# Kernel tuning notes

Measured on AMD Instinct MI355X. Metric: run time of the kernel, lower is better.

The kernel has to match this reference:

```python
import jax, jax.numpy as jnp
import numpy as np

D = 800  # embed dim == GRU units (hardcoded in module)


def gru_scan(x, h0, W, U, b):
    """Keras GRU, reset_after=True, activation=tanh, recurrent_activation=softmax.
    x: [B,T,D_in], h0: [B,H], W: [D_in,3H], U: [H,3H], b: [2,3H] (input bias, recurrent bias).
    Gate order: z, r, h (Keras convention). Returns (seq [B,T,H], last state [B,H])."""
    H = h0.shape[-1]
    # Precompute input projections for all timesteps (big fused GEMM).
    xg = jnp.einsum('btd,dk->btk', x, W) + b[0]          # [B,T,3H]
    xg = jnp.swapaxes(xg, 0, 1)                          # [T,B,3H]
    br = b[1]

    def step(h, xt):
        rec = h @ U + br                                 # [B,3H]
        rz, rr, rh = rec[:, :H], rec[:, H:2 * H], rec[:, 2 * H:]
        xz, xr, xh = xt[:, :H], xt[:, H:2 * H], xt[:, 2 * H:]
        z = jax.nn.softmax(xz + rz, axis=-1)             # recurrent_activation='softmax'
        r = jax.nn.softmax(xr + rr, axis=-1)
        hh = jnp.tanh(xh + r * rh)                       # reset_after: r applied after recurrent matmul
        hn = z * h + (1.0 - z) * hh
        return hn, hn

    hT, ys = jax.lax.scan(step, h0, xg)
    return jnp.swapaxes(ys, 0, 1), hT


def setup_inputs() -> dict:
    key = jax.random.key(0)
    ks = jax.random.split(key, 16)
    Vf, Ve, B, T = 30000, 32000, 64, 48
    s = 0.05

    def n(k, shape):
        return jax.random.normal(k, shape, jnp.float32) * s

    return {
        'encoder_input': jax.random.randint(ks[0], (B, T), 0, Vf),
        'decoder_input': jax.random.randint(ks[1], (B, T), 0, Ve),
        'emb_fr': n(ks[2], (Vf, D)),
        'W_d1': n(ks[3], (D, D)), 'b_d1': jnp.zeros((D,), jnp.float32),
        'Wf1': n(ks[4], (D, 3 * D)), 'Uf1': n(ks[5], (D, 3 * D)), 'bf1': jnp.zeros((2, 3 * D), jnp.float32),
        'Wf2': n(ks[6], (D, 3 * D)), 'Uf2': n(ks[7], (D, 3 * D)), 'bf2': jnp.zeros((2, 3 * D), jnp.float32),
        'emb_en': n(ks[8], (Ve, D)),
        'We1': n(ks[9], (D, 3 * D)), 'Ue1': n(ks[10], (D, 3 * D)), 'be1': jnp.zeros((2, 3 * D), jnp.float32),
        'We2': n(ks[11], (D, 3 * D)), 'Ue2': n(ks[12], (D, 3 * D)), 'be2': jnp.zeros((2, 3 * D), jnp.float32),
        'W_out': n(ks[13], (D, Ve)), 'b_out': jnp.zeros((Ve,), jnp.float32),
    }


def reference(encoder_input, decoder_input, emb_fr, W_d1, b_d1,
              Wf1, Uf1, bf1, Wf2, Uf2, bf2, emb_en,
              We1, Ue1, be1, We2, Ue2, be2, W_out, b_out):
    fe = emb_fr[encoder_input]                           # [B,Tf,D]
    fe = jax.nn.relu(fe @ W_d1 + b_d1)
    ee = emb_en[decoder_input]                           # [B,Te,D]
    B = encoder_input.shape[0]
    h0 = jnp.zeros((B, D), dtype=fe.dtype)
    g1, h1 = gru_scan(fe, h0, Wf1, Uf1, bf1)
    g2, h2 = gru_scan(g1, h1, Wf2, Uf2, bf2)
    e1, h3 = gru_scan(ee, h2, We1, Ue1, be1)
    e2, h4 = gru_scan(e1, h3, We2, Ue2, be2)
    logits = e2 @ W_out + b_out                          # [B,Te,Ve]
    return jax.nn.softmax(logits, axis=-1)
```

## Files before the change

### kernel.cpp

```cpp
#include <hip/hip_runtime.h>

#define DD 800
#define HH 800
#define BB 64
#define TT 48
#define N3H 2400
#define VV 32000
#define MR (TT*BB)
#define NBLK 25

typedef __attribute__((ext_vector_type(8))) short bf16x8;
typedef __attribute__((ext_vector_type(4))) float f32x4;
typedef __attribute__((ext_vector_type(4))) float float4v;
typedef __attribute__((address_space(1))) const unsigned int as1_uint;
typedef __attribute__((address_space(3))) unsigned int as3_uint;

__device__ __forceinline__ short f2bf(float f) {
  unsigned int u = __builtin_bit_cast(unsigned int, f);
  u = (u + 0x7fffu + ((u >> 16) & 1u)) >> 16;
  return (short)(unsigned short)u;
}

__device__ __forceinline__ void gload16(const void* g, void* l) {
  __builtin_amdgcn_global_load_lds((as1_uint*)g, (as3_uint*)l, 16, 0, 0);
}

__device__ __forceinline__ void store16_cc(short* p, bf16x8 v) {
  asm volatile("global_store_dwordx4 %0, %1, off sc0 sc1" :: "v"(p), "v"(v));
}

__global__ void k_cast_transpose(const float* __restrict__ src, short* __restrict__ dst,
                                 int K, int N) {
  __shared__ float tile[32][33];
  int n0 = blockIdx.x * 32, k0 = blockIdx.y * 32;
  int tx = threadIdx.x, ty = threadIdx.y;
#pragma unroll
  for (int i = 0; i < 4; ++i) {
    int k = k0 + ty + i * 8, n = n0 + tx;
    if (k < K && n < N) tile[ty + i * 8][tx] = src[(size_t)k * N + n];
  }
  __syncthreads();
#pragma unroll
  for (int i = 0; i < 4; ++i) {
    int n = n0 + ty + i * 8, k = k0 + tx;
    if (n < N && k < K) dst[(size_t)n * K + k] = f2bf(tile[tx][ty + i * 8]);
  }
}

__global__ void k_gather(const int* __restrict__ ids, const float* __restrict__ emb,
                         short* __restrict__ out) {
  int r = blockIdx.x;
  int t = r >> 6, b = r & 63;
  int id = ids[b * TT + t];
  int i = threadIdx.x;
  if (i < 100) {
    const float* s = emb + (size_t)id * DD + i * 8;
    float4v v0 = *(const float4v*)s;
    float4v v1 = *(const float4v*)(s + 4);
    bf16x8 o;
    o[0] = f2bf(v0[0]); o[1] = f2bf(v0[1]); o[2] = f2bf(v0[2]); o[3] = f2bf(v0[3]);
    o[4] = f2bf(v1[0]); o[5] = f2bf(v1[1]); o[6] = f2bf(v1[2]); o[7] = f2bf(v1[3]);
    *(bf16x8*)(out + (size_t)r * DD + i * 8) = o;
  }
}

template <int EPI>
__global__ __launch_bounds__(256) void k_gemm(const short* __restrict__ A,
                                              const short* __restrict__ BT,
                                              const float* __restrict__ bias,
                                              float* __restrict__ Cf,
                                              short* __restrict__ Cb,
                                              float* __restrict__ Pp,
                                              int N, int K, int ldc) {
  __shared__ short lA[128 * 32];
  __shared__ short lB[128 * 32];
  const int tid = threadIdx.x, wid = tid >> 6, lane = tid & 63;
  const int m0 = blockIdx.y * 128, n0 = blockIdx.x * 128;
  const int wr = wid >> 1, wc = wid & 1;
  f32x4 acc[4][4] = {};
  for (int kt = 0; kt < K / 32; ++kt) {
    const int kb = kt * 32;
#pragma unroll
    for (int rr = 0; rr < 2; ++rr) {
      int s = rr * 256 + tid;
      gload16(A + (size_t)(m0 + (s >> 2)) * K + kb + (s & 3) * 8, (char*)lA + s * 16);
      gload16(BT + (size_t)(n0 + (s >> 2)) * K + kb + (s & 3) * 8, (char*)lB + s * 16);
    }
    __syncthreads();
    bf16x8 af[4], bfr[4];
#pragma unroll
    for (int i = 0; i < 4; ++i)
      af[i] = *(const bf16x8*)(lA + (wr * 64 + i * 16 + (lane & 15)) * 32 + (lane >> 4) * 8);
#pragma unroll
    for (int j = 0; j < 4; ++j)
      bfr[j] = *(const bf16x8*)(lB + (wc * 64 + j * 16 + (lane & 15)) * 32 + (lane >> 4) * 8);
#pragma unroll
    for (int i = 0; i < 4; ++i)
#pragma unroll
      for (int j = 0; j < 4; ++j)
        acc[i][j] = __builtin_amdgcn_mfma_f32_16x16x32_bf16(af[i], bfr[j], acc[i][j], 0, 0, 0);
    __syncthreads();
  }
  const int hi = lane >> 4, ccol = lane & 15;
  if (EPI == 2) {
#pragma unroll
    for (int i = 0; i < 4; ++i) {
      int row = m0 + wr * 64 + i * 16 + hi * 4;
#pragma unroll
      for (int rg = 0; rg < 4; ++rg) {
        int r = row + rg;
        int orow = (r & 63) * TT + (r >> 6);
        float part = 0.f;
#pragma unroll
        for (int j = 0; j < 4; ++j) {
          int col = n0 + wc * 64 + j * 16 + ccol;
          float v = __expf(acc[i][j][rg] + bias[col]);
          part += v;
          Cf[(size_t)orow * ldc + col] = v;
        }
#pragma unroll
        for (int mm = 1; mm < 16; mm <<= 1) part += __shfl_xor(part, mm);
        if (ccol == 0) Pp[(size_t)orow * 512 + blockIdx.x * 2 + wc] = part;
      }
    }
  } else {
#pragma unroll
    for (int i = 0; i < 4; ++i) {
      int row = m0 + wr * 64 + i * 16 + hi * 4;
#pragma unroll
      for (int j = 0; j < 4; ++j) {
        int col = n0 + wc * 64 + j * 16 + ccol;
        if (col >= N) continue;
        float bv = bias ? bias[col] : 0.f;
#pragma unroll
        for (int rg = 0; rg < 4; ++rg) {
          int r = row + rg;
          float v = acc[i][j][rg] + bv;
          if (EPI == 0) Cf[(size_t)r * ldc + col] = v;
          else          Cb[(size_t)r * ldc + col] = f2bf(v < 0.f ? 0.f : v);
        }
      }
    }
  }
}

__device__ __forceinline__ void bar_sync(int* flags, int ep, int tid) {
  asm volatile("s_waitcnt vmcnt(0)" ::: "memory");
  __syncthreads();
  if (tid == 0)
    __hip_atomic_store(&flags[blockIdx.x * 32], ep, __ATOMIC_RELAXED, __HIP_MEMORY_SCOPE_AGENT);
  if (tid < 64) {
    bool ok;
    do {
      int v = ep;
      if (tid < NBLK)
        v = __hip_atomic_load(&flags[tid * 32], __ATOMIC_RELAXED, __HIP_MEMORY_SCOPE_AGENT);
      ok = __all(v - ep >= 0);
      if (!ok) __builtin_amdgcn_s_sleep(1);
    } while (!ok);
  }
  __syncthreads();
}

__global__ __launch_bounds__(512, 1) void k_scan(const float* __restrict__ xg,
                                                 const short* __restrict__ UT,
                                                 const float* __restrict__ br,
                                                 float* __restrict__ hF,
                                                 const short* __restrict__ hInit,
                                                 short* __restrict__ hSeq,
                                                 float* __restrict__ Spart,
                                                 int* flags, int ep0) {
  __shared__ short uT[96 * 808];
  __shared__ float sSum[128];
  __shared__ short hTile[64 * 32];
  const int tid = threadIdx.x, wid = tid >> 6, lane = tid & 63;
  const int bid = blockIdx.x, c0 = bid * 32;
  const int rt = wid & 3, ch = wid >> 2;
  for (int idx = tid; idx < 96 * 100; idx += 512) {
    int rr = idx / 100, chk = idx % 100;
    int grow = (rr >> 5) * HH + c0 + (rr & 31);
    *(bf16x8*)(uT + rr * 808 + chk * 8) = *(const bf16x8*)(UT + (size_t)grow * HH + chk * 8);
  }
  const int hi = lane >> 4;
  const int ccol = lane & 15;
  const int crow = rt * 16 + hi * 4;
  const int gcol = c0 + ch * 16 + ccol;
  const int arow = rt * 16 + ccol;
  const short* uz = uT + (0 * 32 + ch * 16 + ccol) * 808;
  const short* ur = uT + (1 * 32 + ch * 16 + ccol) * 808;
  const short* uh = uT + (2 * 32 + ch * 16 + ccol) * 808;
  f32x4 hfr;
#pragma unroll
  for (int rg = 0; rg < 4; ++rg) hfr[rg] = hF[(crow + rg) * HH + gcol];
  const float brz = br[gcol], brr = br[HH + gcol], brh = br[2 * HH + gcol];
  int ep = ep0;
  float xzv[4], xrv[4], xhv[4];
#pragma unroll
  for (int rg = 0; rg < 4; ++rg) {
    const float* xrow = xg + ((size_t)(crow + rg)) * N3H;
    xzv[rg] = xrow[gcol];
    xrv[rg] = xrow[HH + gcol];
    xhv[rg] = xrow[2 * HH + gcol];
  }
  __syncthreads();

#pragma unroll 1
  for (int t = 0; t < TT; ++t) {
    const short* hPrev = (t == 0) ? hInit : hSeq + (size_t)(t - 1) * BB * HH;
    bf16x8 areg[25];
#pragma unroll
    for (int kt = 0; kt < 25; ++kt)
      areg[kt] = *(const bf16x8*)(hPrev + arow * HH + kt * 32 + hi * 8);
    f32x4 az = {}, ar = {}, ah = {};
#pragma unroll
    for (int kt = 0; kt < 25; ++kt) {
      const int o = kt * 32 + hi * 8;
      az = __builtin_amdgcn_mfma_f32_16x16x32_bf16(areg[kt], *(const bf16x8*)(uz + o), az, 0, 0, 0);
      ar = __builtin_amdgcn_mfma_f32_16x16x32_bf16(areg[kt], *(const bf16x8*)(ur + o), ar, 0, 0, 0);
      ah = __builtin_amdgcn_mfma_f32_16x16x32_bf16(areg[kt], *(const bf16x8*)(uh + o), ah, 0, 0, 0);
    }
    float ez[4], er[4], rh[4];
    float* sb = Spart + (size_t)t * 50 * 128;
#pragma unroll
    for (int rg = 0; rg < 4; ++rg) {
      ez[rg] = __expf(xzv[rg] + az[rg] + brz);
      er[rg] = __expf(xrv[rg] + ar[rg] + brr);
      rh[rg] = ah[rg] + brh;
      float s1 = ez[rg], s2 = er[rg];
#pragma unroll
      for (int mm = 1; mm < 16; mm <<= 1) {
        s1 += __shfl_xor(s1, mm);
        s2 += __shfl_xor(s2, mm);
      }
      if (ccol == 0) {
        const int slot = bid * 2 + ch;
        __hip_atomic_store(&sb[slot * 128 + crow + rg], s1, __ATOMIC_RELAXED, __HIP_MEMORY_SCOPE_AGENT);
        __hip_atomic_store(&sb[slot * 128 + 64 + crow + rg], s2, __ATOMIC_RELAXED, __HIP_MEMORY_SCOPE_AGENT);
      }
    }
    bar_sync(flags, ++ep, tid);
    if (tid < 128) {
      float s = 0.f;
#pragma unroll
      for (int sl = 0; sl < 2 * NBLK; ++sl)
        s += __hip_atomic_load(&sb[sl * 128 + tid], __ATOMIC_RELAXED, __HIP_MEMORY_SCOPE_AGENT);
      sSum[tid] = s;
    }
    __syncthreads();
#pragma unroll
    for (int rg = 0; rg < 4; ++rg) {
      int r = crow + rg;
      float z = ez[rg] / sSum[r];
      float rr2 = er[rg] / sSum[64 + r];
      float hh = tanhf(xhv[rg] + rr2 * rh[rg]);
      float hn = z * hfr[rg] + (1.f - z) * hh;
      hfr[rg] = hn;
      hTile[r * 32 + ch * 16 + ccol] = f2bf(hn);
    }
    __syncthreads();
    short* hCur = hSeq + (size_t)t * BB * HH;
    if (tid < 256) {
      int row = tid >> 2, seg = tid & 3;
      store16_cc(hCur + row * HH + c0 + seg * 8, *(const bf16x8*)(hTile + row * 32 + seg * 8));
    }
    if (t + 1 < TT) {
#pragma unroll
      for (int rg = 0; rg < 4; ++rg) {
        const float* xrow = xg + ((size_t)(t + 1) * BB + crow + rg) * N3H;
        xzv[rg] = xrow[gcol];
        xrv[rg] = xrow[HH + gcol];
        xhv[rg] = xrow[2 * HH + gcol];
      }
    }
    bar_sync(flags, ++ep, tid);
  }
#pragma unroll
  for (int rg = 0; rg < 4; ++rg) hF[(crow + rg) * HH + gcol] = hfr[rg];
}

__global__ __launch_bounds__(256) void k_softmax(float* __restrict__ out,
                                                 const float* __restrict__ Pp) {
  float* row = out + (size_t)blockIdx.x * VV;
  const float* pp = Pp + (size_t)blockIdx.x * 512;
  const int tid = threadIdx.x;
  __shared__ float red[4];
  float sum = 0.f;
  for (int i = tid; i < 500; i += 256) sum += pp[i];
#pragma unroll
  for (int s = 32; s >= 1; s >>= 1) sum += __shfl_xor(sum, s);
  if ((tid & 63) == 0) red[tid >> 6] = sum;
  __syncthreads();
  float inv = 1.f / (red[0] + red[1] + red[2] + red[3]);
  for (int i = tid * 4; i < VV; i += 1024) {
    float4v v = *(const float4v*)(row + i);
    v[0] *= inv; v[1] *= inv; v[2] *= inv; v[3] *= inv;
    *(float4v*)(row + i) = v;
  }
}

extern "C" void kernel_launch(void* const* d_in, const int* in_sizes, int n_in,
                              void* d_out, int out_size, void* d_ws, size_t ws_size,
                              hipStream_t stream) {
  (void)in_sizes; (void)n_in; (void)out_size; (void)ws_size;
  const int*   enc  = (const int*)d_in[0];
  const int*   dec  = (const int*)d_in[1];
  const float* embF = (const float*)d_in[2];
  const float* Wd1  = (const float*)d_in[3];
  const float* bd1  = (const float*)d_in[4];
  const float* Wf1  = (const float*)d_in[5];
  const float* Uf1  = (const float*)d_in[6];
  const float* bf1  = (const float*)d_in[7];
  const float* Wf2  = (const float*)d_in[8];
  const float* Uf2  = (const float*)d_in[9];
  const float* bf2  = (const float*)d_in[10];
  const float* embE = (const float*)d_in[11];
  const float* We1  = (const float*)d_in[12];
  const float* Ue1  = (const float*)d_in[13];
  const float* be1  = (const float*)d_in[14];
  const float* We2  = (const float*)d_in[15];
  const float* Ue2  = (const float*)d_in[16];
  const float* be2  = (const float*)d_in[17];
  const float* Wout = (const float*)d_in[18];
  const float* bout = (const float*)d_in[19];

  char* p = (char*)d_ws;
  auto alloc = [&](size_t bytes) { char* r = p; p += (bytes + 255) & ~(size_t)255; return r; };
  short* WdT = (short*)alloc((size_t)896 * 800 * 2);
  short* WTb[4]; short* UTb[4];
  for (int i = 0; i < 4; ++i) {
    WTb[i] = (short*)alloc((size_t)2432 * 800 * 2);
    UTb[i] = (short*)alloc((size_t)2400 * 800 * 2);
  }
  short* WoT = (short*)alloc((size_t)VV * 800 * 2);
  short* feA = (short*)alloc((size_t)MR * DD * 2);
  short* fe  = (short*)alloc((size_t)MR * DD * 2);
  short* ee  = (short*)alloc((size_t)MR * DD * 2);
  short* g1  = (short*)alloc((size_t)MR * HH * 2);
  short* g2s = (short*)alloc((size_t)MR * HH * 2);
  short* e1  = (short*)alloc((size_t)MR * HH * 2);
  short* e2  = (short*)alloc((size_t)MR * HH * 2);
  float* xg  = (float*)alloc((size_t)MR * N3H * 4);
  float* Ppart = (float*)alloc((size_t)MR * 512 * 4);
  float* Spart = (float*)alloc((size_t)TT * 50 * 128 * 4);
  float* hF   = (float*)alloc((size_t)BB * HH * 4);
  short* hIn0 = (short*)alloc((size_t)BB * HH * 2);
  int* flags  = (int*)alloc((size_t)NBLK * 32 * 4);

  size_t tail = (char*)(flags + NBLK * 32) - (char*)hF;
  hipMemsetAsync(hF, 0, tail, stream);

  dim3 tb(32, 8);
  k_cast_transpose<<<dim3(25, 25), tb, 0, stream>>>(Wd1, WdT, 800, 800);
  const float* Ws[4] = {Wf1, Wf2, We1, We2};
  const float* Us[4] = {Uf1, Uf2, Ue1, Ue2};
  for (int i = 0; i < 4; ++i) {
    k_cast_transpose<<<dim3(75, 25), tb, 0, stream>>>(Ws[i], WTb[i], 800, 2400);
    k_cast_transpose<<<dim3(75, 25), tb, 0, stream>>>(Us[i], UTb[i], 800, 2400);
  }
  k_cast_transpose<<<dim3(1000, 25), tb, 0, stream>>>(Wout, WoT, 800, VV);
  k_gather<<<MR, 128, 0, stream>>>(enc, embF, feA);
  k_gather<<<MR, 128, 0, stream>>>(dec, embE, ee);
  k_gemm<1><<<dim3(7, 24), 256, 0, stream>>>(feA, WdT, bd1, nullptr, fe, nullptr, 800, 800, 800);

  const float* bs[4] = {bf1, bf2, be1, be2};
  const short* Xs[4] = {fe, g1, ee, e1};
  short* hSeqL[4] = {g1, g2s, e1, e2};
  for (int l = 0; l < 4; ++l) {
    const short* hInit = (l == 0) ? hIn0 : hSeqL[l - 1] + (size_t)(TT - 1) * BB * HH;
    k_gemm<0><<<dim3(19, 24), 256, 0, stream>>>(Xs[l], WTb[l], bs[l], xg, nullptr, nullptr, N3H, 800, N3H);
    k_scan<<<NBLK, 512, 0, stream>>>(xg, UTb[l], bs[l] + N3H, hF, hInit, hSeqL[l],
                                     Spart, flags, l * 2 * TT);
  }
  k_gemm<2><<<dim3(250, 24), 256, 0, stream>>>(e2, WoT, bout, (float*)d_out, nullptr, Ppart, VV, 800, VV);
  k_softmax<<<MR, 256, 0, stream>>>((float*)d_out, Ppart);
}
```

Measured before the change: 2.525 ms.

## Replace block-wide grid barriers with per-row-tile wave-level flag synchronization in GRU scan

Each wave in the recurrent scan kernel now owns one 16-row batch tile and syncs only with the 50 waves across blocks that share that tile, using per-slot flags, instead of block-wide __syncthreads plus a grid barrier. Softmax partial sums are exchanged per row tile and reduced in-wave with shuffles, which removes the shared-memory sum and h-tile staging. Hidden state is written directly with per-element coherent short stores. The aim is to cut barrier latency on the serial time-step critical path, at the cost of more polling traffic and narrower, uncoalesced h stores.

Result: slower. 3.883 ms (+53.8%).

```diff
diff --git a/kernel.cpp b/kernel.cpp
--- a/kernel.cpp
+++ b/kernel.cpp
@@ -25,8 +25,11 @@
   __builtin_amdgcn_global_load_lds((as1_uint*)g, (as3_uint*)l, 16, 0, 0);
 }
 
-__device__ __forceinline__ void store16_cc(short* p, bf16x8 v) {
-  asm volatile("global_store_dwordx4 %0, %1, off sc0 sc1" :: "v"(p), "v"(v));
+__device__ __forceinline__ void storef_cc(float* p, float v) {
+  asm volatile("global_store_dword %0, %1, off sc0 sc1" :: "v"(p), "v"(v));
+}
+__device__ __forceinline__ void stores_cc(short* p, int v) {
+  asm volatile("global_store_short %0, %1, off sc0 sc1" :: "v"(p), "v"(v));
 }
 
 __global__ void k_cast_transpose(const float* __restrict__ src, short* __restrict__ dst,
@@ -144,22 +147,16 @@
   }
 }
 
-__device__ __forceinline__ void bar_sync(int* flags, int ep, int tid) {
-  asm volatile("s_waitcnt vmcnt(0)" ::: "memory");
-  __syncthreads();
-  if (tid == 0)
-    __hip_atomic_store(&flags[blockIdx.x * 32], ep, __ATOMIC_RELAXED, __HIP_MEMORY_SCOPE_AGENT);
-  if (tid < 64) {
-    bool ok;
-    do {
-      int v = ep;
-      if (tid < NBLK)
-        v = __hip_atomic_load(&flags[tid * 32], __ATOMIC_RELAXED, __HIP_MEMORY_SCOPE_AGENT);
-      ok = __all(v - ep >= 0);
-      if (!ok) __builtin_amdgcn_s_sleep(1);
-    } while (!ok);
-  }
-  __syncthreads();
+__device__ __forceinline__ void wait_flags(int* fl, int tgt, int lane) {
+  bool ok;
+  do {
+    int v = tgt;
+    if (lane < 2 * NBLK)
+      v = __hip_atomic_load(&fl[lane], __ATOMIC_RELAXED, __HIP_MEMORY_SCOPE_AGENT);
+    ok = __all(v - tgt >= 0);
+    if (!ok) __builtin_amdgcn_s_sleep(1);
+  } while (!ok);
+  asm volatile("" ::: "memory");
 }
 
 __global__ __launch_bounds__(512, 1) void k_scan(const float* __restrict__ xg,
@@ -168,14 +165,12 @@
                                                  float* __restrict__ hF,
                                                  const short* __restrict__ hInit,
                                                  short* __restrict__ hSeq,
-                                                 float* __restrict__ Spart,
-                                                 int* flags, int ep0) {
+                                                 float* __restrict__ Sp,
+                                                 int* __restrict__ flags, int ep0) {
   __shared__ short uT[96 * 808];
-  __shared__ float sSum[128];
-  __shared__ short hTile[64 * 32];
   const int tid = threadIdx.x, wid = tid >> 6, lane = tid & 63;
   const int bid = blockIdx.x, c0 = bid * 32;
-  const int rt = wid & 3, ch = wid >> 2;
+  const int rt = wid >> 1, ch = wid & 1;
   for (int idx = tid; idx < 96 * 100; idx += 512) {
     int rr = idx / 100, chk = idx % 100;
     int grow = (rr >> 5) * HH + c0 + (rr & 31);
@@ -183,17 +178,19 @@
   }
   const int hi = lane >> 4;
   const int ccol = lane & 15;
-  const int crow = rt * 16 + hi * 4;
+  const int lrow = hi * 4;
+  const int crow = rt * 16 + lrow;
   const int gcol = c0 + ch * 16 + ccol;
   const int arow = rt * 16 + ccol;
   const short* uz = uT + (0 * 32 + ch * 16 + ccol) * 808;
   const short* ur = uT + (1 * 32 + ch * 16 + ccol) * 808;
   const short* uh = uT + (2 * 32 + ch * 16 + ccol) * 808;
+  int* fl = flags + rt * 64;
+  const int slot = bid * 2 + ch;
   f32x4 hfr;
 #pragma unroll
   for (int rg = 0; rg < 4; ++rg) hfr[rg] = hF[(crow + rg) * HH + gcol];
   const float brz = br[gcol], brr = br[HH + gcol], brh = br[2 * HH + gcol];
-  int ep = ep0;
   float xzv[4], xrv[4], xhv[4];
 #pragma unroll
   for (int rg = 0; rg < 4; ++rg) {
@@ -220,7 +217,7 @@
       ah = __builtin_amdgcn_mfma_f32_16x16x32_bf16(areg[kt], *(const bf16x8*)(uh + o), ah, 0, 0, 0);
     }
     float ez[4], er[4], rh[4];
-    float* sb = Spart + (size_t)t * 50 * 128;
+    float* sb = Sp + ((size_t)(t * 4 + rt) * 2 * NBLK + slot) * 32;
 #pragma unroll
     for (int rg = 0; rg < 4; ++rg) {
       ez[rg] = __expf(xzv[rg] + az[rg] + brz);
@@ -233,36 +230,35 @@
         s2 += __shfl_xor(s2, mm);
       }
       if (ccol == 0) {
-        const int slot = bid * 2 + ch;
-        __hip_atomic_store(&sb[slot * 128 + crow + rg], s1, __ATOMIC_RELAXED, __HIP_MEMORY_SCOPE_AGENT);
-        __hip_atomic_store(&sb[slot * 128 + 64 + crow + rg], s2, __ATOMIC_RELAXED, __HIP_MEMORY_SCOPE_AGENT);
-      }
-    }
-    bar_sync(flags, ++ep, tid);
-    if (tid < 128) {
-      float s = 0.f;
-#pragma unroll
-      for (int sl = 0; sl < 2 * NBLK; ++sl)
-        s += __hip_atomic_load(&sb[sl * 128 + tid], __ATOMIC_RELAXED, __HIP_MEMORY_SCOPE_AGENT);
-      sSum[tid] = s;
-    }
-    __syncthreads();
+        storef_cc(&sb[lrow + rg], s1);
+        storef_cc(&sb[16 + lrow + rg], s2);
+      }
+    }
+    asm volatile("s_waitcnt vmcnt(0)" ::: "memory");
+    if (lane == 0)
+      __hip_atomic_store(&fl[slot], ep0 + 2 * t + 1, __ATOMIC_RELAXED, __HIP_MEMORY_SCOPE_AGENT);
+    wait_flags(fl, ep0 + 2 * t + 1, lane);
+    const int sidx = lane & 31, half = lane >> 5;
+    const float* sd = Sp + ((size_t)(t * 4 + rt) * 2 * NBLK + half * NBLK) * 32 + sidx;
+    float ps = 0.f;
+#pragma unroll
+    for (int k = 0; k < NBLK; ++k) ps += sd[k * 32];
+    ps += __shfl_xor(ps, 32);
+    short* hCur = hSeq + (size_t)t * BB * HH;
 #pragma unroll
     for (int rg = 0; rg < 4; ++rg) {
-      int r = crow + rg;
-      float z = ez[rg] / sSum[r];
-      float rr2 = er[rg] / sSum[64 + r];
+      float zden = __shfl(ps, lrow + rg);
+      float rden = __shfl(ps, 16 + lrow + rg);
+      float z = ez[rg] / zden;
+      float rr2 = er[rg] / rden;
       float hh = tanhf(xhv[rg] + rr2 * rh[rg]);
       float hn = z * hfr[rg] + (1.f - z) * hh;
       hfr[rg] = hn;
-      hTile[r * 32 + ch * 16 + ccol] = f2bf(hn);
-    }
-    __syncthreads();
-    short* hCur = hSeq + (size_t)t * BB * HH;
-    if (tid < 256) {
-      int row = tid >> 2, seg = tid & 3;
-      store16_cc(hCur + row * HH + c0 + seg * 8, *(const bf16x8*)(hTile + row * 32 + seg * 8));
-    }
+      stores_cc(&hCur[(crow + rg) * HH + gcol], (int)(unsigned short)f2bf(hn));
+    }
+    asm volatile("s_waitcnt vmcnt(0)" ::: "memory");
+    if (lane == 0)
+      __hip_atomic_store(&fl[slot], ep0 + 2 * t + 2, __ATOMIC_RELAXED, __HIP_MEMORY_SCOPE_AGENT);
     if (t + 1 < TT) {
 #pragma unroll
       for (int rg = 0; rg < 4; ++rg) {
@@ -271,8 +267,8 @@
         xrv[rg] = xrow[HH + gcol];
         xhv[rg] = xrow[2 * HH + gcol];
       }
-    }
-    bar_sync(flags, ++ep, tid);
+      wait_flags(fl, ep0 + 2 * t + 2, lane);
+    }
   }
 #pragma unroll
   for (int rg = 0; rg < 4; ++rg) hF[(crow + rg) * HH + gcol] = hfr[rg];
@@ -341,12 +337,12 @@
   short* e2  = (short*)alloc((size_t)MR * HH * 2);
   float* xg  = (float*)alloc((size_t)MR * N3H * 4);
   float* Ppart = (float*)alloc((size_t)MR * 512 * 4);
-  float* Spart = (float*)alloc((size_t)TT * 50 * 128 * 4);
+  float* Spart = (float*)alloc((size_t)4 * TT * 4 * 2 * NBLK * 32 * 4);
   float* hF   = (float*)alloc((size_t)BB * HH * 4);
   short* hIn0 = (short*)alloc((size_t)BB * HH * 2);
-  int* flags  = (int*)alloc((size_t)NBLK * 32 * 4);
-
-  size_t tail = (char*)(flags + NBLK * 32) - (char*)hF;
+  int* flags  = (int*)alloc((size_t)4 * 64 * 4);
+
+  size_t tail = (char*)(flags + 4 * 64) - (char*)hF;
   hipMemsetAsync(hF, 0, tail, stream);
 
   dim3 tb(32, 8);
@@ -369,7 +365,8 @@
     const short* hInit = (l == 0) ? hIn0 : hSeqL[l - 1] + (size_t)(TT - 1) * BB * HH;
     k_gemm<0><<<dim3(19, 24), 256, 0, stream>>>(Xs[l], WTb[l], bs[l], xg, nullptr, nullptr, N3H, 800, N3H);
     k_scan<<<NBLK, 512, 0, stream>>>(xg, UTb[l], bs[l] + N3H, hF, hInit, hSeqL[l],
-                                     Spart, flags, l * 2 * TT);
+                                     Spart + (size_t)l * TT * 4 * 2 * NBLK * 32,
+                                     flags, l * 2 * TT);
   }
   k_gemm<2><<<dim3(250, 24), 256, 0, stream>>>(e2, WoT, bout, (float*)d_out, nullptr, Ppart, VV, 800, VV);
   k_softmax<<<MR, 256, 0, stream>>>((float*)d_out, Ppart);
```

## Co-locate scan blocks on one XCC and use L2-local barriers

Applied to the files above, without the earlier changes.

The scan kernel now launches 256 blocks. Each block reads its XCC id and registers through atomics, and the first XCC to collect 25 blocks is elected; only those blocks do the recurrence, with a role index in place of blockIdx. Because every participant shares one L2, the cross-block flags, partial softmax sums and hidden-state stores switch from agent-scope/system-coherent (sc0 sc1) stores to plain stores and L2-level atomic reads, cutting barrier latency per timestep. This relies on undocumented co-residency assumptions, namely that 25 blocks land on one XCC and that plain stores are visible across CUs via L2. It adds bounded spin guards that could silently break synchronization if they time out.

After: 2.885 ms. 1.14x slower.

```diff
diff --git a/kernel.cpp b/kernel.cpp
--- a/kernel.cpp
+++ b/kernel.cpp
@@ -25,8 +25,13 @@
   __builtin_amdgcn_global_load_lds((as1_uint*)g, (as3_uint*)l, 16, 0, 0);
 }
 
-__device__ __forceinline__ void store16_cc(short* p, bf16x8 v) {
-  asm volatile("global_store_dwordx4 %0, %1, off sc0 sc1" :: "v"(p), "v"(v));
+__device__ __forceinline__ int atomic_read_l2(int* p) {
+  int v;
+  int zero = 0;
+  asm volatile("global_atomic_add %0, %1, %2, off sc0"
+               : "=&v"(v) : "v"(p), "v"(zero) : "memory");
+  asm volatile("s_waitcnt vmcnt(0)");
+  return v;
 }
 
 __global__ void k_cast_transpose(const float* __restrict__ src, short* __restrict__ dst,
@@ -144,20 +149,20 @@
   }
 }
 
-__device__ __forceinline__ void bar_sync(int* flags, int ep, int tid) {
+__device__ __forceinline__ void bar_sync(int* flags, int ep, int tid, int role) {
   asm volatile("s_waitcnt vmcnt(0)" ::: "memory");
   __syncthreads();
-  if (tid == 0)
-    __hip_atomic_store(&flags[blockIdx.x * 32], ep, __ATOMIC_RELAXED, __HIP_MEMORY_SCOPE_AGENT);
+  if (tid == 0) flags[role * 16] = ep;
   if (tid < 64) {
     bool ok;
+    int guard = 0;
     do {
       int v = ep;
-      if (tid < NBLK)
-        v = __hip_atomic_load(&flags[tid * 32], __ATOMIC_RELAXED, __HIP_MEMORY_SCOPE_AGENT);
+      if (tid < NBLK) v = atomic_read_l2(&flags[tid * 16]);
       ok = __all(v - ep >= 0);
-      if (!ok) __builtin_amdgcn_s_sleep(1);
-    } while (!ok);
+      if (!ok) __builtin_amdgcn_s_sleep(2);
+    } while (!ok && ++guard < (1 << 18));
+    asm volatile("" ::: "memory");
   }
   __syncthreads();
 }
@@ -168,13 +173,36 @@
                                                  float* __restrict__ hF,
                                                  const short* __restrict__ hInit,
                                                  short* __restrict__ hSeq,
-                                                 float* __restrict__ Spart,
-                                                 int* flags, int ep0) {
+                                                 float* __restrict__ Sp,
+                                                 int* __restrict__ flags, int ep0,
+                                                 int* __restrict__ xreg) {
+  __shared__ int sRole;
+  if (threadIdx.x == 0) {
+    int xcc;
+    asm volatile("s_getreg_b32 %0, hwreg(HW_REG_XCC_ID)" : "=s"(xcc));
+    xcc &= 7;
+    int r = __hip_atomic_fetch_add(&xreg[xcc], 1, __ATOMIC_RELAXED, __HIP_MEMORY_SCOPE_AGENT);
+    if (r == NBLK - 1) {
+      int exp0 = 0;
+      __hip_atomic_compare_exchange_strong(&xreg[8], &exp0, xcc + 1, __ATOMIC_RELAXED,
+                                           __ATOMIC_RELAXED, __HIP_MEMORY_SCOPE_AGENT);
+    }
+    int w, guard = 0;
+    do {
+      w = __hip_atomic_load(&xreg[8], __ATOMIC_RELAXED, __HIP_MEMORY_SCOPE_AGENT);
+      if (w == 0) __builtin_amdgcn_s_sleep(2);
+    } while (w == 0 && ++guard < (1 << 20));
+    sRole = (w != 0 && xcc == w - 1 && r < NBLK) ? r : -1;
+  }
+  __syncthreads();
+  const int role = sRole;
+  if (role < 0) return;
+
   __shared__ short uT[96 * 808];
   __shared__ float sSum[128];
   __shared__ short hTile[64 * 32];
   const int tid = threadIdx.x, wid = tid >> 6, lane = tid & 63;
-  const int bid = blockIdx.x, c0 = bid * 32;
+  const int c0 = role * 32;
   const int rt = wid & 3, ch = wid >> 2;
   for (int idx = tid; idx < 96 * 100; idx += 512) {
     int rr = idx / 100, chk = idx % 100;
@@ -220,7 +248,7 @@
       ah = __builtin_amdgcn_mfma_f32_16x16x32_bf16(areg[kt], *(const bf16x8*)(uh + o), ah, 0, 0, 0);
     }
     float ez[4], er[4], rh[4];
-    float* sb = Spart + (size_t)t * 50 * 128;
+    float* sb = Sp + (size_t)t * 50 * 128;
 #pragma unroll
     for (int rg = 0; rg < 4; ++rg) {
       ez[rg] = __expf(xzv[rg] + az[rg] + brz);
@@ -233,17 +261,16 @@
         s2 += __shfl_xor(s2, mm);
       }
       if (ccol == 0) {
-        const int slot = bid * 2 + ch;
-        __hip_atomic_store(&sb[slot * 128 + crow + rg], s1, __ATOMIC_RELAXED, __HIP_MEMORY_SCOPE_AGENT);
-        __hip_atomic_store(&sb[slot * 128 + 64 + crow + rg], s2, __ATOMIC_RELAXED, __HIP_MEMORY_SCOPE_AGENT);
+        const int slot = role * 2 + ch;
+        sb[slot * 128 + crow + rg] = s1;
+        sb[slot * 128 + 64 + crow + rg] = s2;
       }
     }
-    bar_sync(flags, ++ep, tid);
+    bar_sync(flags, ++ep, tid, role);
     if (tid < 128) {
       float s = 0.f;
 #pragma unroll
-      for (int sl = 0; sl < 2 * NBLK; ++sl)
-        s += __hip_atomic_load(&sb[sl * 128 + tid], __ATOMIC_RELAXED, __HIP_MEMORY_SCOPE_AGENT);
+      for (int sl = 0; sl < 2 * NBLK; ++sl) s += sb[sl * 128 + tid];
       sSum[tid] = s;
     }
     __syncthreads();
@@ -261,7 +288,7 @@
     short* hCur = hSeq + (size_t)t * BB * HH;
     if (tid < 256) {
       int row = tid >> 2, seg = tid & 3;
-      store16_cc(hCur + row * HH + c0 + seg * 8, *(const bf16x8*)(hTile + row * 32 + seg * 8));
+      *(bf16x8*)(hCur + row * HH + c0 + seg * 8) = *(const bf16x8*)(hTile + row * 32 + seg * 8);
     }
     if (t + 1 < TT) {
 #pragma unroll
@@ -272,7 +299,7 @@
         xhv[rg] = xrow[2 * HH + gcol];
       }
     }
-    bar_sync(flags, ++ep, tid);
+    bar_sync(flags, ++ep, tid, role);
   }
 #pragma unroll
   for (int rg = 0; rg < 4; ++rg) hF[(crow + rg) * HH + gcol] = hfr[rg];
@@ -341,12 +368,13 @@
   short* e2  = (short*)alloc((size_t)MR * HH * 2);
   float* xg  = (float*)alloc((size_t)MR * N3H * 4);
   float* Ppart = (float*)alloc((size_t)MR * 512 * 4);
-  float* Spart = (float*)alloc((size_t)TT * 50 * 128 * 4);
+  float* Spart = (float*)alloc((size_t)4 * TT * 50 * 128 * 4);
   float* hF   = (float*)alloc((size_t)BB * HH * 4);
   short* hIn0 = (short*)alloc((size_t)BB * HH * 2);
-  int* flags  = (int*)alloc((size_t)NBLK * 32 * 4);
-
-  size_t tail = (char*)(flags + NBLK * 32) - (char*)hF;
+  int* flags  = (int*)alloc((size_t)NBLK * 16 * 4);
+  int* xreg   = (int*)alloc((size_t)4 * 16 * 4);
+
+  size_t tail = (char*)(xreg + 4 * 16) - (char*)hF;
   hipMemsetAsync(hF, 0, tail, stream);
 
   dim3 tb(32, 8);
@@ -368,8 +396,9 @@
   for (int l = 0; l < 4; ++l) {
     const short* hInit = (l == 0) ? hIn0 : hSeqL[l - 1] + (size_t)(TT - 1) * BB * HH;
     k_gemm<0><<<dim3(19, 24), 256, 0, stream>>>(Xs[l], WTb[l], bs[l], xg, nullptr, nullptr, N3H, 800, N3H);
-    k_scan<<<NBLK, 512, 0, stream>>>(xg, UTb[l], bs[l] + N3H, hF, hInit, hSeqL[l],
-                                     Spart, flags, l * 2 * TT);
+    k_scan<<<256, 512, 0, stream>>>(xg, UTb[l], bs[l] + N3H, hF, hInit, hSeqL[l],
+                                    Spart + (size_t)l * TT * 50 * 128,
+                                    flags, l * 2 * TT, xreg + l * 16);
   }
   k_gemm<2><<<dim3(250, 24), 256, 0, stream>>>(e2, WoT, bout, (float*)d_out, nullptr, Ppart, VV, 800, VV);
   k_softmax<<<MR, 256, 0, stream>>>((float*)d_out, Ppart);
```

## Overlap next-layer input GEMM with GRU scan in a persistent fused kernel

Applied to the files above, without the earlier changes.

The scan and the following GEMM are merged into one persistent kernel. The first 25 blocks run the recurrent scan while the remaining blocks pull GEMM tiles from an atomic counter. Each GEMM tile first polls the scan's per-block epoch flags until the rows of hidden states it needs have been written. This overlaps the next layer's input projection, and finally the output-vocabulary GEMM, with the latency-bound recurrence, using double-buffered xg storage. The risks are contention between the spin-waiting GEMM blocks and the scan blocks, and correctness that depends on the flag and memory ordering. For the layer-2 GEMM on decoder embeddings, the poll is disabled.

Measured after the change: 2.369 ms. 6.2% less time.

```diff
diff --git a/kernel.cpp b/kernel.cpp
--- a/kernel.cpp
+++ b/kernel.cpp
@@ -70,7 +70,6 @@
                                               const float* __restrict__ bias,
                                               float* __restrict__ Cf,
                                               short* __restrict__ Cb,
-                                              float* __restrict__ Pp,
                                               int N, int K, int ldc) {
   __shared__ short lA[128 * 32];
   __shared__ short lB[128 * 32];
@@ -102,43 +101,20 @@
     __syncthreads();
   }
   const int hi = lane >> 4, ccol = lane & 15;
-  if (EPI == 2) {
-#pragma unroll
-    for (int i = 0; i < 4; ++i) {
-      int row = m0 + wr * 64 + i * 16 + hi * 4;
+#pragma unroll
+  for (int i = 0; i < 4; ++i) {
+    int row = m0 + wr * 64 + i * 16 + hi * 4;
+#pragma unroll
+    for (int j = 0; j < 4; ++j) {
+      int col = n0 + wc * 64 + j * 16 + ccol;
+      if (col >= N) continue;
+      float bv = bias ? bias[col] : 0.f;
 #pragma unroll
       for (int rg = 0; rg < 4; ++rg) {
         int r = row + rg;
-        int orow = (r & 63) * TT + (r >> 6);
-        float part = 0.f;
-#pragma unroll
-        for (int j = 0; j < 4; ++j) {
-          int col = n0 + wc * 64 + j * 16 + ccol;
-          float v = __expf(acc[i][j][rg] + bias[col]);
-          part += v;
-          Cf[(size_t)orow * ldc + col] = v;
-        }
-#pragma unroll
-        for (int mm = 1; mm < 16; mm <<= 1) part += __shfl_xor(part, mm);
-        if (ccol == 0) Pp[(size_t)orow * 512 + blockIdx.x * 2 + wc] = part;
-      }
-    }
-  } else {
-#pragma unroll
-    for (int i = 0; i < 4; ++i) {
-      int row = m0 + wr * 64 + i * 16 + hi * 4;
-#pragma unroll
-      for (int j = 0; j < 4; ++j) {
-        int col = n0 + wc * 64 + j * 16 + ccol;
-        if (col >= N) continue;
-        float bv = bias ? bias[col] : 0.f;
-#pragma unroll
-        for (int rg = 0; rg < 4; ++rg) {
-          int r = row + rg;
-          float v = acc[i][j][rg] + bv;
-          if (EPI == 0) Cf[(size_t)r * ldc + col] = v;
-          else          Cb[(size_t)r * ldc + col] = f2bf(v < 0.f ? 0.f : v);
-        }
+        float v = acc[i][j][rg] + bv;
+        if (EPI == 0) Cf[(size_t)r * ldc + col] = v;
+        else          Cb[(size_t)r * ldc + col] = f2bf(v < 0.f ? 0.f : v);
       }
     }
   }
@@ -162,120 +138,210 @@
   __syncthreads();
 }
 
-__global__ __launch_bounds__(512, 1) void k_scan(const float* __restrict__ xg,
-                                                 const short* __restrict__ UT,
-                                                 const float* __restrict__ br,
-                                                 float* __restrict__ hF,
-                                                 const short* __restrict__ hInit,
-                                                 short* __restrict__ hSeq,
-                                                 float* __restrict__ Spart,
-                                                 int* flags, int ep0) {
-  __shared__ short uT[96 * 808];
-  __shared__ float sSum[128];
-  __shared__ short hTile[64 * 32];
+template <int HEPI>
+__global__ __launch_bounds__(512, 1) void k_fused(
+    const float* __restrict__ xg, const short* __restrict__ UT,
+    const float* __restrict__ br, float* __restrict__ hF,
+    const short* __restrict__ hInit, short* __restrict__ hSeq,
+    float* __restrict__ Spart, int* __restrict__ flags, int ep0,
+    const short* __restrict__ gA, const short* __restrict__ gBT,
+    const float* __restrict__ gbias, float* __restrict__ gCf,
+    float* __restrict__ gPp, int gN, int gldc, int gNT, int gNtiles,
+    int* __restrict__ tcnt, int pollBase) {
+  __shared__ __align__(16) char smem[159744];
   const int tid = threadIdx.x, wid = tid >> 6, lane = tid & 63;
-  const int bid = blockIdx.x, c0 = bid * 32;
-  const int rt = wid & 3, ch = wid >> 2;
-  for (int idx = tid; idx < 96 * 100; idx += 512) {
-    int rr = idx / 100, chk = idx % 100;
-    int grow = (rr >> 5) * HH + c0 + (rr & 31);
-    *(bf16x8*)(uT + rr * 808 + chk * 8) = *(const bf16x8*)(UT + (size_t)grow * HH + chk * 8);
-  }
-  const int hi = lane >> 4;
-  const int ccol = lane & 15;
-  const int crow = rt * 16 + hi * 4;
-  const int gcol = c0 + ch * 16 + ccol;
-  const int arow = rt * 16 + ccol;
-  const short* uz = uT + (0 * 32 + ch * 16 + ccol) * 808;
-  const short* ur = uT + (1 * 32 + ch * 16 + ccol) * 808;
-  const short* uh = uT + (2 * 32 + ch * 16 + ccol) * 808;
-  f32x4 hfr;
-#pragma unroll
-  for (int rg = 0; rg < 4; ++rg) hfr[rg] = hF[(crow + rg) * HH + gcol];
-  const float brz = br[gcol], brr = br[HH + gcol], brh = br[2 * HH + gcol];
-  int ep = ep0;
-  float xzv[4], xrv[4], xhv[4];
-#pragma unroll
-  for (int rg = 0; rg < 4; ++rg) {
-    const float* xrow = xg + ((size_t)(crow + rg)) * N3H;
-    xzv[rg] = xrow[gcol];
-    xrv[rg] = xrow[HH + gcol];
-    xhv[rg] = xrow[2 * HH + gcol];
-  }
-  __syncthreads();
+  const int hi = lane >> 4, ccol = lane & 15;
+
+  if (blockIdx.x < NBLK) {
+    short* uT    = (short*)smem;
+    float* sSum  = (float*)(smem + 155136);
+    short* hTile = (short*)(smem + 155648);
+    const int bid = blockIdx.x, c0 = bid * 32;
+    const int rt = wid & 3, ch = wid >> 2;
+    for (int idx = tid; idx < 96 * 100; idx += 512) {
+      int rr = idx / 100, chk = idx % 100;
+      int grow = (rr >> 5) * HH + c0 + (rr & 31);
+      *(bf16x8*)(uT + rr * 808 + chk * 8) = *(const bf16x8*)(UT + (size_t)grow * HH + chk * 8);
+    }
+    const int crow = rt * 16 + hi * 4;
+    const int gcol = c0 + ch * 16 + ccol;
+    const int arow = rt * 16 + ccol;
+    const short* uz = uT + (0 * 32 + ch * 16 + ccol) * 808;
+    const short* ur = uT + (1 * 32 + ch * 16 + ccol) * 808;
+    const short* uh = uT + (2 * 32 + ch * 16 + ccol) * 808;
+    f32x4 hfr;
+#pragma unroll
+    for (int rg = 0; rg < 4; ++rg) hfr[rg] = hF[(crow + rg) * HH + gcol];
+    const float brz = br[gcol], brr = br[HH + gcol], brh = br[2 * HH + gcol];
+    int ep = ep0;
+    float xzv[4], xrv[4], xhv[4];
+#pragma unroll
+    for (int rg = 0; rg < 4; ++rg) {
+      const float* xrow = xg + ((size_t)(crow + rg)) * N3H;
+      xzv[rg] = xrow[gcol];
+      xrv[rg] = xrow[HH + gcol];
+      xhv[rg] = xrow[2 * HH + gcol];
+    }
+    __syncthreads();
 
 #pragma unroll 1
-  for (int t = 0; t < TT; ++t) {
-    const short* hPrev = (t == 0) ? hInit : hSeq + (size_t)(t - 1) * BB * HH;
-    bf16x8 areg[25];
-#pragma unroll
-    for (int kt = 0; kt < 25; ++kt)
-      areg[kt] = *(const bf16x8*)(hPrev + arow * HH + kt * 32 + hi * 8);
-    f32x4 az = {}, ar = {}, ah = {};
-#pragma unroll
+    for (int t = 0; t < TT; ++t) {
+      const short* hPrev = (t == 0) ? hInit : hSeq + (size_t)(t - 1) * BB * HH;
+      bf16x8 areg[25];
+#pragma unroll
+      for (int kt = 0; kt < 25; ++kt)
+        areg[kt] = *(const bf16x8*)(hPrev + arow * HH + kt * 32 + hi * 8);
+      f32x4 az = {}, ar = {}, ah = {};
+#pragma unroll
+      for (int kt = 0; kt < 25; ++kt) {
+        const int o = kt * 32 + hi * 8;
+        az = __builtin_amdgcn_mfma_f32_16x16x32_bf16(areg[kt], *(const bf16x8*)(uz + o), az, 0, 0, 0);
+        ar = __builtin_amdgcn_mfma_f32_16x16x32_bf16(areg[kt], *(const bf16x8*)(ur + o), ar, 0, 0, 0);
+        ah = __builtin_amdgcn_mfma_f32_16x16x32_bf16(areg[kt], *(const bf16x8*)(uh + o), ah, 0, 0, 0);
+      }
+      float ez[4], er[4], rh[4];
+      float* sb = Spart + (size_t)t * 50 * 128;
+#pragma unroll
+      for (int rg = 0; rg < 4; ++rg) {
+        ez[rg] = __expf(xzv[rg] + az[rg] + brz);
+        er[rg] = __expf(xrv[rg] + ar[rg] + brr);
+        rh[rg] = ah[rg] + brh;
+        float s1 = ez[rg], s2 = er[rg];
+#pragma unroll
+        for (int mm = 1; mm < 16; mm <<= 1) {
+          s1 += __shfl_xor(s1, mm);
+          s2 += __shfl_xor(s2, mm);
+        }
+        if (ccol == 0) {
+          const int slot = bid * 2 + ch;
+          __hip_atomic_store(&sb[slot * 128 + crow + rg], s1, __ATOMIC_RELAXED, __HIP_MEMORY_SCOPE_AGENT);
+          __hip_atomic_store(&sb[slot * 128 + 64 + crow + rg], s2, __ATOMIC_RELAXED, __HIP_MEMORY_SCOPE_AGENT);
+        }
+      }
+      bar_sync(flags, ++ep, tid);
+      if (tid < 128) {
+        float s = 0.f;
+#pragma unroll
+        for (int sl = 0; sl < 2 * NBLK; ++sl)
+          s += __hip_atomic_load(&sb[sl * 128 + tid], __ATOMIC_RELAXED, __HIP_MEMORY_SCOPE_AGENT);
+        sSum[tid] = s;
+      }
+      __syncthreads();
+#pragma unroll
+      for (int rg = 0; rg < 4; ++rg) {
+        int r = crow + rg;
+        float z = ez[rg] / sSum[r];
+        float rr2 = er[rg] / sSum[64 + r];
+        float hh = tanhf(xhv[rg] + rr2 * rh[rg]);
+        float hn = z * hfr[rg] + (1.f - z) * hh;
+        hfr[rg] = hn;
+        hTile[r * 32 + ch * 16 + ccol] = f2bf(hn);
+      }
+      __syncthreads();
+      short* hCur = hSeq + (size_t)t * BB * HH;
+      if (tid < 256) {
+        int row = tid >> 2, seg = tid & 3;
+        store16_cc(hCur + row * HH + c0 + seg * 8, *(const bf16x8*)(hTile + row * 32 + seg * 8));
+      }
+      if (t + 1 < TT) {
+#pragma unroll
+        for (int rg = 0; rg < 4; ++rg) {
+          const float* xrow = xg + ((size_t)(t + 1) * BB + crow + rg) * N3H;
+          xzv[rg] = xrow[gcol];
+          xrv[rg] = xrow[HH + gcol];
+          xhv[rg] = xrow[2 * HH + gcol];
+        }
+      }
+      bar_sync(flags, ++ep, tid);
+    }
+#pragma unroll
+    for (int rg = 0; rg < 4; ++rg) hF[(crow + rg) * HH + gcol] = hfr[rg];
+    return;
+  }
+
+  short* lA = (short*)smem;
+  short* lB = (short*)(smem + 8192);
+  int*   tk = (int*)(smem + 16384);
+  const int wr = wid >> 1, wc = wid & 1;
+  for (;;) {
+    if (tid == 0)
+      tk[0] = __hip_atomic_fetch_add(tcnt, 1, __ATOMIC_RELAXED, __HIP_MEMORY_SCOPE_AGENT);
+    __syncthreads();
+    const int t0 = tk[0];
+    if (t0 >= gNtiles) break;
+    const int mb = t0 / gNT, nb = t0 % gNT;
+    const int m0 = mb * 128, n0 = nb * 128;
+    {
+      int tmax = 2 * mb + 1; if (tmax > TT - 1) tmax = TT - 1;
+      const int ft = pollBase + 2 * tmax + 2;
+      bool ok;
+      do {
+        int v = ft;
+        if (lane < NBLK)
+          v = __hip_atomic_load(&flags[lane * 32], __ATOMIC_RELAXED, __HIP_MEMORY_SCOPE_AGENT);
+        ok = __all(v - ft >= 0);
+        if (!ok) __builtin_amdgcn_s_sleep(2);
+      } while (!ok);
+      asm volatile("" ::: "memory");
+    }
+    f32x4 acc[2][4] = {};
+    const int srow = tid >> 2, sseg = tid & 3;
     for (int kt = 0; kt < 25; ++kt) {
-      const int o = kt * 32 + hi * 8;
-      az = __builtin_amdgcn_mfma_f32_16x16x32_bf16(areg[kt], *(const bf16x8*)(uz + o), az, 0, 0, 0);
-      ar = __builtin_amdgcn_mfma_f32_16x16x32_bf16(areg[kt], *(const bf16x8*)(ur + o), ar, 0, 0, 0);
-      ah = __builtin_amdgcn_mfma_f32_16x16x32_bf16(areg[kt], *(const bf16x8*)(uh + o), ah, 0, 0, 0);
-    }
-    float ez[4], er[4], rh[4];
-    float* sb = Spart + (size_t)t * 50 * 128;
-#pragma unroll
-    for (int rg = 0; rg < 4; ++rg) {
-      ez[rg] = __expf(xzv[rg] + az[rg] + brz);
-      er[rg] = __expf(xrv[rg] + ar[rg] + brr);
-      rh[rg] = ah[rg] + brh;
-      float s1 = ez[rg], s2 = er[rg];
-#pragma unroll
-      for (int mm = 1; mm < 16; mm <<= 1) {
-        s1 += __shfl_xor(s1, mm);
-        s2 += __shfl_xor(s2, mm);
-      }
-      if (ccol == 0) {
-        const int slot = bid * 2 + ch;
-        __hip_atomic_store(&sb[slot * 128 + crow + rg], s1, __ATOMIC_RELAXED, __HIP_MEMORY_SCOPE_AGENT);
-        __hip_atomic_store(&sb[slot * 128 + 64 + crow + rg], s2, __ATOMIC_RELAXED, __HIP_MEMORY_SCOPE_AGENT);
-      }
-    }
-    bar_sync(flags, ++ep, tid);
-    if (tid < 128) {
-      float s = 0.f;
-#pragma unroll
-      for (int sl = 0; sl < 2 * NBLK; ++sl)
-        s += __hip_atomic_load(&sb[sl * 128 + tid], __ATOMIC_RELAXED, __HIP_MEMORY_SCOPE_AGENT);
-      sSum[tid] = s;
-    }
-    __syncthreads();
-#pragma unroll
-    for (int rg = 0; rg < 4; ++rg) {
-      int r = crow + rg;
-      float z = ez[rg] / sSum[r];
-      float rr2 = er[rg] / sSum[64 + r];
-      float hh = tanhf(xhv[rg] + rr2 * rh[rg]);
-      float hn = z * hfr[rg] + (1.f - z) * hh;
-      hfr[rg] = hn;
-      hTile[r * 32 + ch * 16 + ccol] = f2bf(hn);
-    }
-    __syncthreads();
-    short* hCur = hSeq + (size_t)t * BB * HH;
-    if (tid < 256) {
-      int row = tid >> 2, seg = tid & 3;
-      store16_cc(hCur + row * HH + c0 + seg * 8, *(const bf16x8*)(hTile + row * 32 + seg * 8));
-    }
-    if (t + 1 < TT) {
-#pragma unroll
-      for (int rg = 0; rg < 4; ++rg) {
-        const float* xrow = xg + ((size_t)(t + 1) * BB + crow + rg) * N3H;
-        xzv[rg] = xrow[gcol];
-        xrv[rg] = xrow[HH + gcol];
-        xhv[rg] = xrow[2 * HH + gcol];
-      }
-    }
-    bar_sync(flags, ++ep, tid);
-  }
-#pragma unroll
-  for (int rg = 0; rg < 4; ++rg) hF[(crow + rg) * HH + gcol] = hfr[rg];
+      const int kb = kt * 32;
+      gload16(gA + (size_t)(m0 + srow) * 800 + kb + sseg * 8, (char*)lA + tid * 16);
+      gload16(gBT + (size_t)(n0 + srow) * 800 + kb + sseg * 8, (char*)lB + tid * 16);
+      __syncthreads();
+      bf16x8 af[2], bf[4];
+#pragma unroll
+      for (int i = 0; i < 2; ++i)
+        af[i] = *(const bf16x8*)(lA + (wr * 32 + i * 16 + (lane & 15)) * 32 + hi * 8);
+#pragma unroll
+      for (int j = 0; j < 4; ++j)
+        bf[j] = *(const bf16x8*)(lB + (wc * 64 + j * 16 + (lane & 15)) * 32 + hi * 8);
+#pragma unroll
+      for (int i = 0; i < 2; ++i)
+#pragma unroll
+        for (int j = 0; j < 4; ++j)
+          acc[i][j] = __builtin_amdgcn_mfma_f32_16x16x32_bf16(af[i], bf[j], acc[i][j], 0, 0, 0);
+      __syncthreads();
+    }
+    if (HEPI == 2) {
+#pragma unroll
+      for (int i = 0; i < 2; ++i) {
+        int row = m0 + wr * 32 + i * 16 + hi * 4;
+#pragma unroll
+        for (int rg = 0; rg < 4; ++rg) {
+          int r = row + rg;
+          int orow = (r & 63) * TT + (r >> 6);
+          float part = 0.f;
+#pragma unroll
+          for (int j = 0; j < 4; ++j) {
+            int col = n0 + wc * 64 + j * 16 + ccol;
+            float v = __expf(acc[i][j][rg] + gbias[col]);
+            part += v;
+            gCf[(size_t)orow * gldc + col] = v;
+          }
+#pragma unroll
+          for (int mm = 1; mm < 16; mm <<= 1) part += __shfl_xor(part, mm);
+          if (ccol == 0) gPp[(size_t)orow * 512 + nb * 2 + wc] = part;
+        }
+      }
+    } else {
+#pragma unroll
+      for (int i = 0; i < 2; ++i) {
+        int row = m0 + wr * 32 + i * 16 + hi * 4;
+#pragma unroll
+        for (int j = 0; j < 4; ++j) {
+          int col = n0 + wc * 64 + j * 16 + ccol;
+          if (col >= gN) continue;
+          float bv = gbias[col];
+#pragma unroll
+          for (int rg = 0; rg < 4; ++rg)
+            gCf[(size_t)(row + rg) * gldc + col] = acc[i][j][rg] + bv;
+        }
+      }
+    }
+  }
 }
 
 __global__ __launch_bounds__(256) void k_softmax(float* __restrict__ out,
@@ -339,14 +405,16 @@
   short* g2s = (short*)alloc((size_t)MR * HH * 2);
   short* e1  = (short*)alloc((size_t)MR * HH * 2);
   short* e2  = (short*)alloc((size_t)MR * HH * 2);
-  float* xg  = (float*)alloc((size_t)MR * N3H * 4);
+  float* xgA = (float*)alloc((size_t)MR * N3H * 4);
+  float* xgB = (float*)alloc((size_t)MR * N3H * 4);
   float* Ppart = (float*)alloc((size_t)MR * 512 * 4);
   float* Spart = (float*)alloc((size_t)TT * 50 * 128 * 4);
   float* hF   = (float*)alloc((size_t)BB * HH * 4);
   short* hIn0 = (short*)alloc((size_t)BB * HH * 2);
   int* flags  = (int*)alloc((size_t)NBLK * 32 * 4);
-
-  size_t tail = (char*)(flags + NBLK * 32) - (char*)hF;
+  int* tcnt   = (int*)alloc((size_t)16 * 4);
+
+  size_t tail = (char*)(tcnt + 16) - (char*)hF;
   hipMemsetAsync(hF, 0, tail, stream);
 
   dim3 tb(32, 8);
@@ -360,17 +428,31 @@
   k_cast_transpose<<<dim3(1000, 25), tb, 0, stream>>>(Wout, WoT, 800, VV);
   k_gather<<<MR, 128, 0, stream>>>(enc, embF, feA);
   k_gather<<<MR, 128, 0, stream>>>(dec, embE, ee);
-  k_gemm<1><<<dim3(7, 24), 256, 0, stream>>>(feA, WdT, bd1, nullptr, fe, nullptr, 800, 800, 800);
+  k_gemm<1><<<dim3(7, 24), 256, 0, stream>>>(feA, WdT, bd1, nullptr, fe, 800, 800, 800);
+  k_gemm<0><<<dim3(19, 24), 256, 0, stream>>>(fe, WTb[0], bf1, xgA, nullptr, N3H, 800, N3H);
 
   const float* bs[4] = {bf1, bf2, be1, be2};
-  const short* Xs[4] = {fe, g1, ee, e1};
   short* hSeqL[4] = {g1, g2s, e1, e2};
+  float* xgR[4] = {xgA, xgB, xgA, xgB};
+  const short* hA[4]   = {g1, ee, e1, e2};
+  const short* hBT[4]  = {WTb[1], WTb[2], WTb[3], WoT};
+  const float* hBias[4]= {bs[1], bs[2], bs[3], bout};
+  float* hOut[4] = {xgB, xgA, xgB, (float*)d_out};
+  int   hPoll[4] = {0 * 96, -1000000, 2 * 96, 3 * 96};
+
   for (int l = 0; l < 4; ++l) {
     const short* hInit = (l == 0) ? hIn0 : hSeqL[l - 1] + (size_t)(TT - 1) * BB * HH;
-    k_gemm<0><<<dim3(19, 24), 256, 0, stream>>>(Xs[l], WTb[l], bs[l], xg, nullptr, nullptr, N3H, 800, N3H);
-    k_scan<<<NBLK, 512, 0, stream>>>(xg, UTb[l], bs[l] + N3H, hF, hInit, hSeqL[l],
-                                     Spart, flags, l * 2 * TT);
-  }
-  k_gemm<2><<<dim3(250, 24), 256, 0, stream>>>(e2, WoT, bout, (float*)d_out, nullptr, Ppart, VV, 800, VV);
+    if (l < 3) {
+      k_fused<0><<<256, 512, 0, stream>>>(xgR[l], UTb[l], bs[l] + N3H, hF, hInit, hSeqL[l],
+                                          Spart, flags, l * 2 * TT,
+                                          hA[l], hBT[l], hBias[l], hOut[l], nullptr,
+                                          N3H, N3H, 19, 24 * 19, &tcnt[l], hPoll[l]);
+    } else {
+      k_fused<2><<<256, 512, 0, stream>>>(xgR[l], UTb[l], bs[l] + N3H, hF, hInit, hSeqL[l],
+                                          Spart, flags, l * 2 * TT,
+                                          hA[l], hBT[l], hBias[l], hOut[l], Ppart,
+                                          VV, VV, 250, 24 * 250, &tcnt[l], hPoll[l]);
+    }
+  }
   k_softmax<<<MR, 256, 0, stream>>>((float*)d_out, Ppart);
 }
```
